# Kernel optimization log

Measured on AMD Instinct MI355X. Metric: run time of the kernel, lower is better.

## Reference

```python
import jax, jax.numpy as jnp
import numpy as np

N_NODES = 100000
N_EDGES = 1600000
IN_FEATS = 128
HIDDEN = 128
N_CLASSES = 47


def setup_inputs() -> dict:
    key = jax.random.key(0)
    ks = jax.random.split(key, 8)
    x = jax.random.normal(ks[0], (N_NODES, IN_FEATS), dtype=jnp.float32)
    edges = jax.random.randint(ks[1], (2, N_EDGES), 0, N_NODES, dtype=jnp.int32)
    W0 = jax.random.normal(ks[2], (IN_FEATS, HIDDEN), dtype=jnp.float32) * (1.0 / np.sqrt(IN_FEATS))
    b0 = jnp.zeros((HIDDEN,), dtype=jnp.float32)
    W1 = jax.random.normal(ks[3], (HIDDEN, HIDDEN), dtype=jnp.float32) * (1.0 / np.sqrt(HIDDEN))
    b1 = jnp.zeros((HIDDEN,), dtype=jnp.float32)
    Wc = jax.random.normal(ks[4], (HIDDEN, N_CLASSES), dtype=jnp.float32) * (1.0 / np.sqrt(HIDDEN))
    bc = jnp.zeros((N_CLASSES,), dtype=jnp.float32)
    return {"x": x, "edges": edges, "W0": W0, "b0": b0, "W1": W1, "b1": b1, "Wc": Wc, "bc": bc}


def reference(x, edges, W0, b0, W1, b1, Wc, bc):
    N = x.shape[0]
    src, dst = edges[0], edges[1]
    ones = jnp.ones((src.shape[0],), dtype=x.dtype)
    # symmetric 'both' normalization: out-degree for src, in-degree for dst (clamped to >=1)
    out_deg = jax.ops.segment_sum(ones, src, num_segments=N)
    in_deg = jax.ops.segment_sum(ones, dst, num_segments=N)
    c_src = jnp.maximum(out_deg, 1.0) ** -0.5  # [N]
    c_dst = jnp.maximum(in_deg, 1.0) ** -0.5   # [N]

    def graph_conv(h, W, b):
        h = (h * c_src[:, None]) @ W                       # dense transform [N, H]
        h = jax.ops.segment_sum(h[src], dst, num_segments=N)  # sparse SpMM aggregation
        h = h * c_dst[:, None] + b
        return jax.nn.relu(h)

    h = graph_conv(x, W0, b0)
    h = graph_conv(h, W1, b1)
    return h @ Wc + bc
```

## Files before the change

### kernel.cpp

```cpp
#include <hip/hip_runtime.h>
#include <hip/hip_fp16.h>


#define PB 256
#define BSHIFT 8

typedef _Float16 f16x8 __attribute__((ext_vector_type(8)));
typedef float f32x4 __attribute__((ext_vector_type(4)));


__global__ __launch_bounds__(256) void k_histo(const int* __restrict__ src, int E, int* __restrict__ dout) {
  int stride = gridDim.x * blockDim.x;
  for (int e = blockIdx.x * blockDim.x + threadIdx.x; e < E; e += stride)
    atomicAdd(&dout[src[e]], 1);
}

__global__ __launch_bounds__(256) void k_coeffs_src(const int* __restrict__ dout, float* __restrict__ c_src, int N) {
  int i = blockIdx.x * blockDim.x + threadIdx.x;
  if (i < N) c_src[i] = rsqrtf((float)max(dout[i], 1));
}


__global__ __launch_bounds__(256) void k_count(const int* __restrict__ dst, int E, int per_blk, int NB,
                                               int* __restrict__ cntT) {
  __shared__ int cnt[512];
  for (int i = threadIdx.x; i < NB; i += 256) cnt[i] = 0;
  __syncthreads();
  int e0 = blockIdx.x * per_blk, e1 = min(E, e0 + per_blk);
  for (int e = e0 + threadIdx.x; e < e1; e += 256) atomicAdd(&cnt[dst[e] >> BSHIFT], 1);
  __syncthreads();
  for (int i = threadIdx.x; i < NB; i += 256) cntT[i * PB + blockIdx.x] = cnt[i];
}

__global__ __launch_bounds__(256) void k_scanblk(const int* __restrict__ cntT, int* __restrict__ offsT,
                                                 int* __restrict__ total) {
  __shared__ int s[256];
  int b = blockIdx.x, t = threadIdx.x;
  int v = cntT[b * PB + t];
  s[t] = v;
  __syncthreads();
  for (int off = 1; off < 256; off <<= 1) {
    int x = (t >= off) ? s[t - off] : 0;
    __syncthreads();
    s[t] += x;
    __syncthreads();
  }
  offsT[b * PB + t] = s[t] - v;
  if (t == 255) total[b] = s[255];
}

__global__ __launch_bounds__(512) void k_scantot(const int* __restrict__ total, int NB, int E,
                                                 int* __restrict__ bbase, int* __restrict__ row_ptr, int N) {
  __shared__ int s[512];
  int t = threadIdx.x;
  int v = (t < NB) ? total[t] : 0;
  s[t] = v;
  __syncthreads();
  for (int off = 1; off < 512; off <<= 1) {
    int x = (t >= off) ? s[t - off] : 0;
    __syncthreads();
    s[t] += x;
    __syncthreads();
  }
  if (t < NB) bbase[t] = s[t] - v;
  if (t == 0) { bbase[NB] = E; row_ptr[N] = E; }
}


__global__ __launch_bounds__(256) void k_partition(const int* __restrict__ src, const int* __restrict__ dst,
                                                   int E, int per_blk, int NB,
                                                   const int* __restrict__ offsT, const int* __restrict__ bbase,
                                                   unsigned* __restrict__ ebuf, int src_bits) {
  __shared__ int cur[512];
  for (int i = threadIdx.x; i < NB; i += 256) cur[i] = bbase[i] + offsT[i * PB + blockIdx.x];
  __syncthreads();
  int e0 = blockIdx.x * per_blk, e1 = min(E, e0 + per_blk);
  for (int e = e0 + threadIdx.x; e < e1; e += 256) {
    int d = dst[e], s = src[e];
    int pos = atomicAdd(&cur[d >> BSHIFT], 1);
    ebuf[pos] = ((unsigned)(d & ((1 << BSHIFT) - 1)) << src_bits) | (unsigned)s;
  }
}


__global__ __launch_bounds__(256) void k_finalize(const unsigned* __restrict__ ebuf, const int* __restrict__ bbase,
                                                  int N, int src_bits, int* __restrict__ row_ptr,
                                                  float* __restrict__ c_dst, int* __restrict__ col_idx) {
  __shared__ int cnt[256];
  __shared__ int s[256];
  __shared__ int cur[256];
  int b = blockIdx.x, t = threadIdx.x;
  int r0 = bbase[b], r1 = bbase[b + 1];
  cnt[t] = 0;
  __syncthreads();
  for (int i = r0 + t; i < r1; i += 256) atomicAdd(&cnt[ebuf[i] >> src_bits], 1);
  __syncthreads();
  int v = cnt[t];
  s[t] = v;
  __syncthreads();
  for (int off = 1; off < 256; off <<= 1) {
    int x = (t >= off) ? s[t - off] : 0;
    __syncthreads();
    s[t] += x;
    __syncthreads();
  }
  int ex = s[t] - v;
  cur[t] = ex;
  int node = (b << BSHIFT) + t;
  if (node < N) {
    row_ptr[node] = r0 + ex;
    c_dst[node] = rsqrtf((float)max(v, 1));
  }
  __syncthreads();
  unsigned smask = (1u << src_bits) - 1u;
  for (int i = r0 + t; i < r1; i += 256) {
    unsigned e = ebuf[i];
    int pos = r0 + atomicAdd(&cur[e >> src_bits], 1);
    col_idx[pos] = (int)((e & smask) << 8);
  }
}


__device__ __forceinline__ f16x8 load_af(const float* arow, int off, float csc) {
  float4 a0 = *(const float4*)(arow + off);
  float4 a1 = *(const float4*)(arow + off + 4);
  f16x8 v;
  v[0] = (_Float16)(a0.x * csc);
  v[1] = (_Float16)(a0.y * csc);
  v[2] = (_Float16)(a0.z * csc);
  v[3] = (_Float16)(a0.w * csc);
  v[4] = (_Float16)(a1.x * csc);
  v[5] = (_Float16)(a1.y * csc);
  v[6] = (_Float16)(a1.z * csc);
  v[7] = (_Float16)(a1.w * csc);
  return v;
}

__device__ __forceinline__ f16x8 load_af(const __half* arow, int off, float csc) {
  f16x8 v = *(const f16x8*)(arow + off);
  _Float16 c = (_Float16)csc;
#pragma unroll
  for (int j = 0; j < 8; j++) v[j] = v[j] * c;
  return v;
}

template <typename AT>
__global__ __launch_bounds__(256) void k_gemm_mfma(const AT* __restrict__ A, const float* __restrict__ W,
                                                   const float* __restrict__ scale, __half* __restrict__ out, int N) {
  __shared__ _Float16 Wt[128][136];
  int t = threadIdx.x;
  {
    int nlow = t & 15;
    int kplow = t >> 4;
#pragma unroll
    for (int j = 0; j < 32; j++) {
      int n = nlow + 16 * (j & 7);
      int kp = kplow + 16 * (j >> 3);
      float w0 = W[(size_t)(2 * kp) * 128 + n];
      float w1 = W[(size_t)(2 * kp + 1) * 128 + n];
      __half2 h2 = __floats2half2_rn(w0, w1);
      *(__half2*)&Wt[n][2 * kp] = h2;
    }
  }
  __syncthreads();

  int wave = t >> 6;
  int lane = t & 63;
  int li = lane & 15;
  int q = lane >> 4;

#pragma unroll
  for (int s2 = 0; s2 < 2; s2++) {
    int m0 = (blockIdx.x * 2 + s2) * 128 + wave * 32;
    if (m0 >= N) break;

    int mrow[2];
    float csc[2];
    bool mok[2];
    const AT* arow[2];
#pragma unroll
    for (int s = 0; s < 2; s++) {
      mrow[s] = m0 + s * 16 + li;
      mok[s] = mrow[s] < N;
      csc[s] = mok[s] ? scale[mrow[s]] : 0.f;
      arow[s] = A + (size_t)(mok[s] ? mrow[s] : 0) * 128;
    }

    f32x4 acc[2][8];
#pragma unroll
    for (int s = 0; s < 2; s++)
#pragma unroll
      for (int nt = 0; nt < 8; nt++) acc[s][nt] = (f32x4){0.f, 0.f, 0.f, 0.f};

#pragma unroll
    for (int kc = 0; kc < 128; kc += 32) {
      f16x8 af[2];
#pragma unroll
      for (int s = 0; s < 2; s++) af[s] = load_af(arow[s], kc + q * 8, csc[s]);
#pragma unroll
      for (int nt = 0; nt < 8; nt++) {
        f16x8 wf = *(const f16x8*)&Wt[nt * 16 + li][kc + q * 8];
        acc[0][nt] = __builtin_amdgcn_mfma_f32_16x16x32_f16(wf, af[0], acc[0][nt], 0, 0, 0);
        acc[1][nt] = __builtin_amdgcn_mfma_f32_16x16x32_f16(wf, af[1], acc[1][nt], 0, 0, 0);
      }
    }

#pragma unroll
    for (int s = 0; s < 2; s++) {
      if (!mok[s]) continue;
      size_t rb = (size_t)mrow[s] * 128;
#pragma unroll
      for (int nt = 0; nt < 8; nt++) {
        __half2 p0 = __floats2half2_rn(acc[s][nt][0], acc[s][nt][1]);
        __half2 p1 = __floats2half2_rn(acc[s][nt][2], acc[s][nt][3]);
        uint2 qv;
        qv.x = *(unsigned*)&p0;
        qv.y = *(unsigned*)&p1;
        *(uint2*)&out[rb + nt * 16 + q * 4] = qv;
      }
    }
  }
}


__device__ __forceinline__ void acc_pair(float4& a, uint2 qa, uint2 qb) {
  __half2 s0 = __hadd2(*(__half2*)&qa.x, *(__half2*)&qb.x);
  __half2 s1 = __hadd2(*(__half2*)&qa.y, *(__half2*)&qb.y);
  float2 f0 = __half22float2(s0);
  float2 f1 = __half22float2(s1);
  a.x += f0.x; a.y += f0.y; a.z += f1.x; a.w += f1.y;
}

__device__ __forceinline__ void acc_one(float4& a, uint2 q) {
  float2 f0 = __half22float2(*(__half2*)&q.x);
  float2 f1 = __half22float2(*(__half2*)&q.y);
  a.x += f0.x; a.y += f0.y; a.z += f1.x; a.w += f1.y;
}

__global__ __launch_bounds__(256) void k_aggregate_h(const __half* __restrict__ hin, const int* __restrict__ rp,
                                                     const int* __restrict__ ci, const float* __restrict__ c_dst,
                                                     const float* __restrict__ bias, __half* __restrict__ hout, int N) {
  int v = blockIdx.x * 4 + (threadIdx.x >> 6);
  if (v >= N) return;
  int half_id = (threadIdx.x >> 5) & 1;
  int f4 = (threadIdx.x & 31) * 4;
  const char* hb = (const char*)hin + f4 * 2;
  int p0 = rp[v], pe = rp[v + 1];
  int mid = p0 + ((pe - p0 + 1) >> 1);
  int p = half_id ? mid : p0;
  int pend = half_id ? pe : mid;
  float4 a0 = make_float4(0.f, 0.f, 0.f, 0.f);
  float4 a1 = make_float4(0.f, 0.f, 0.f, 0.f);
  float4 a2 = make_float4(0.f, 0.f, 0.f, 0.f);
  float4 a3 = make_float4(0.f, 0.f, 0.f, 0.f);
  for (; p + 7 < pend; p += 8) {
    int u0 = ci[p];
    int u1 = ci[p + 1];
    int u2 = ci[p + 2];
    int u3 = ci[p + 3];
    int u4 = ci[p + 4];
    int u5 = ci[p + 5];
    int u6 = ci[p + 6];
    int u7 = ci[p + 7];
    uint2 q0 = *(const uint2*)(hb + (size_t)(unsigned)u0);
    uint2 q1 = *(const uint2*)(hb + (size_t)(unsigned)u1);
    uint2 q2 = *(const uint2*)(hb + (size_t)(unsigned)u2);
    uint2 q3 = *(const uint2*)(hb + (size_t)(unsigned)u3);
    uint2 q4 = *(const uint2*)(hb + (size_t)(unsigned)u4);
    uint2 q5 = *(const uint2*)(hb + (size_t)(unsigned)u5);
    uint2 q6 = *(const uint2*)(hb + (size_t)(unsigned)u6);
    uint2 q7 = *(const uint2*)(hb + (size_t)(unsigned)u7);
    acc_pair(a0, q0, q1);
    acc_pair(a1, q2, q3);
    acc_pair(a2, q4, q5);
    acc_pair(a3, q6, q7);
  }
  for (; p + 1 < pend; p += 2) {
    int u0 = ci[p];
    int u1 = ci[p + 1];
    uint2 q0 = *(const uint2*)(hb + (size_t)(unsigned)u0);
    uint2 q1 = *(const uint2*)(hb + (size_t)(unsigned)u1);
    acc_pair(a0, q0, q1);
  }
  if (p < pend) {
    uint2 q = *(const uint2*)(hb + (size_t)(unsigned)ci[p]);
    acc_one(a0, q);
  }
  a0.x += a1.x; a0.y += a1.y; a0.z += a1.z; a0.w += a1.w;
  a2.x += a3.x; a2.y += a3.y; a2.z += a3.z; a2.w += a3.w;
  a0.x += a2.x; a0.y += a2.y; a0.z += a2.z; a0.w += a2.w;
  a0.x += __shfl_xor(a0.x, 32);
  a0.y += __shfl_xor(a0.y, 32);
  a0.z += __shfl_xor(a0.z, 32);
  a0.w += __shfl_xor(a0.w, 32);
  if (half_id == 0) {
    float cd = c_dst[v];
    float4 b = *(const float4*)&bias[f4];
    float4 o;
    o.x = fmaxf(fmaf(a0.x, cd, b.x), 0.f);
    o.y = fmaxf(fmaf(a0.y, cd, b.y), 0.f);
    o.z = fmaxf(fmaf(a0.z, cd, b.z), 0.f);
    o.w = fmaxf(fmaf(a0.w, cd, b.w), 0.f);
    __half2 p0h = __floats2half2_rn(o.x, o.y);
    __half2 p1h = __floats2half2_rn(o.z, o.w);
    uint2 qv;
    qv.x = *(unsigned*)&p0h;
    qv.y = *(unsigned*)&p1h;
    *(uint2*)&hout[(size_t)v * 128 + f4] = qv;
  }
}


__global__ __launch_bounds__(256) void k_classifier(const __half* __restrict__ h, const float* __restrict__ Wc,
                                                    const float* __restrict__ bc, float* __restrict__ out, int N) {
  __shared__ float hs[256][33];
  __shared__ float Ws[32][48];
  __shared__ float bs[48];
  int t = threadIdx.x;
  int row0 = blockIdx.x * 256;
  int tc = t & 3;
  int tm = t >> 2;
  if (t < 47) bs[t] = bc[t];
  if (t == 255) bs[47] = 0.f;

  float acc[4][12];
#pragma unroll
  for (int g = 0; g < 4; g++)
#pragma unroll
    for (int j = 0; j < 12; j++) acc[g][j] = 0.f;

  for (int kb = 0; kb < 128; kb += 32) {
#pragma unroll
    for (int i = 0; i < 4; i++) {
      int f = t + i * 256;
      int r = f >> 2;
      int c8 = (f & 3) * 8;
      int g = row0 + r;
      f16x8 v;
      if (g < N) v = *(const f16x8*)&h[(size_t)g * 128 + kb + c8];
      else {
#pragma unroll
        for (int j = 0; j < 8; j++) v[j] = (_Float16)0.f;
      }
#pragma unroll
      for (int j = 0; j < 8; j++) hs[r][c8 + j] = (float)v[j];
    }
#pragma unroll
    for (int i = 0; i < 6; i++) {
      int f = t + i * 256;
      int k = f / 48;
      int c = f - k * 48;
      Ws[k][c] = (c < 47) ? Wc[(size_t)(kb + k) * 47 + c] : 0.f;
    }
    __syncthreads();
#pragma unroll 4
    for (int k = 0; k < 32; k++) {
      float4 w0 = *(const float4*)&Ws[k][tc * 12];
      float4 w1 = *(const float4*)&Ws[k][tc * 12 + 4];
      float4 w2 = *(const float4*)&Ws[k][tc * 12 + 8];
      float a0 = hs[tm][k];
      float a1 = hs[tm + 64][k];
      float a2 = hs[tm + 128][k];
      float a3 = hs[tm + 192][k];
      float a[4] = {a0, a1, a2, a3};
#pragma unroll
      for (int g = 0; g < 4; g++) {
        acc[g][0] = fmaf(a[g], w0.x, acc[g][0]);
        acc[g][1] = fmaf(a[g], w0.y, acc[g][1]);
        acc[g][2] = fmaf(a[g], w0.z, acc[g][2]);
        acc[g][3] = fmaf(a[g], w0.w, acc[g][3]);
        acc[g][4] = fmaf(a[g], w1.x, acc[g][4]);
        acc[g][5] = fmaf(a[g], w1.y, acc[g][5]);
        acc[g][6] = fmaf(a[g], w1.z, acc[g][6]);
        acc[g][7] = fmaf(a[g], w1.w, acc[g][7]);
        acc[g][8] = fmaf(a[g], w2.x, acc[g][8]);
        acc[g][9] = fmaf(a[g], w2.y, acc[g][9]);
        acc[g][10] = fmaf(a[g], w2.z, acc[g][10]);
        acc[g][11] = fmaf(a[g], w2.w, acc[g][11]);
      }
    }
    __syncthreads();
  }
#pragma unroll
  for (int g = 0; g < 4; g++) {
    int r = row0 + tm + 64 * g;
    if (r < N) {
#pragma unroll
      for (int j = 0; j < 12; j++) {
        int c = tc * 12 + j;
        if (c < 47) out[(size_t)r * 47 + c] = acc[g][j] + bs[c];
      }
    }
  }
}


extern "C" void kernel_launch(void* const* d_in, const int* in_sizes, int n_in,
                              void* d_out, int out_size, void* d_ws, size_t ws_size,
                              hipStream_t stream) {
  const float* x  = (const float*)d_in[0];
  const int* edges = (const int*)d_in[1];
  const float* W0 = (const float*)d_in[2];
  const float* b0 = (const float*)d_in[3];
  const float* W1 = (const float*)d_in[4];
  const float* b1 = (const float*)d_in[5];
  const float* Wc = (const float*)d_in[6];
  const float* bc = (const float*)d_in[7];
  float* out = (float*)d_out;

  int N = in_sizes[0] / 128;
  int E = in_sizes[1] / 2;
  const int* src = edges;
  const int* dst = edges + E;

  int NB = (N + ((1 << BSHIFT) - 1)) >> BSHIFT;
  int src_bits = 0;
  while ((1 << src_bits) < N) src_bits++;
  int per_blk = (E + PB - 1) / PB;

  char* base = (char*)d_ws;
  size_t off = 0;
  auto alloc = [&](size_t bytes) -> void* {
    void* p = base + off;
    off += (bytes + 255) & ~(size_t)255;
    return p;
  };
  float* c_src = (float*)alloc((size_t)N * 4);
  float* c_dst = (float*)alloc((size_t)N * 4);
  int* deg_out = (int*)alloc((size_t)N * 4);
  int* row_ptr = (int*)alloc((size_t)(N + 1) * 4);
  int* col_idx = (int*)alloc((size_t)E * 4);
  __half* h0h = (__half*)alloc((size_t)N * 128 * 2);
  __half* h1h = (__half*)alloc((size_t)N * 128 * 2);

  char* hb = (char*)h1h;
  unsigned* ebuf = (unsigned*)hb;            hb += (size_t)E * 4;
  int* cntT = (int*)hb;                      hb += (size_t)NB * PB * 4;
  int* offsT = (int*)hb;                     hb += (size_t)NB * PB * 4;
  int* total = (int*)hb;                     hb += (size_t)NB * 4;
  int* bbase = (int*)hb;                     hb += (size_t)(NB + 1) * 4;

  hipMemsetAsync(deg_out, 0, (size_t)N * 4, stream);
  k_histo<<<1024, 256, 0, stream>>>(src, E, deg_out);
  k_coeffs_src<<<(N + 255) / 256, 256, 0, stream>>>(deg_out, c_src, N);

  k_count<<<PB, 256, 0, stream>>>(dst, E, per_blk, NB, cntT);
  k_scanblk<<<NB, 256, 0, stream>>>(cntT, offsT, total);
  k_scantot<<<1, 512, 0, stream>>>(total, NB, E, bbase, row_ptr, N);
  k_partition<<<PB, 256, 0, stream>>>(src, dst, E, per_blk, NB, offsT, bbase, ebuf, src_bits);
  k_finalize<<<NB, 256, 0, stream>>>(ebuf, bbase, N, src_bits, row_ptr, c_dst, col_idx);

  int strips = (N + 127) / 128;
  int gblocks = (strips + 1) / 2;
  k_gemm_mfma<float><<<gblocks, 256, 0, stream>>>(x, W0, c_src, h0h, N);
  k_aggregate_h<<<(N + 3) / 4, 256, 0, stream>>>(h0h, row_ptr, col_idx, c_dst, b0, h1h, N);
  k_gemm_mfma<__half><<<gblocks, 256, 0, stream>>>(h1h, W1, c_src, h0h, N);
  k_aggregate_h<<<(N + 3) / 4, 256, 0, stream>>>(h0h, row_ptr, col_idx, c_dst, b1, h1h, N);
  k_classifier<<<(N + 255) / 256, 256, 0, stream>>>(h1h, Wc, bc, out, N);
}
```

Baseline: 409.4 us.

## Compute out-degree via bucketed partition instead of global atomic histogram

```diff
diff --git a/kernel.cpp b/kernel.cpp
--- a/kernel.cpp
+++ b/kernel.cpp
@@ -9,27 +9,23 @@
 typedef float f32x4 __attribute__((ext_vector_type(4)));
 
 
-__global__ __launch_bounds__(256) void k_histo(const int* __restrict__ src, int E, int* __restrict__ dout) {
-  int stride = gridDim.x * blockDim.x;
-  for (int e = blockIdx.x * blockDim.x + threadIdx.x; e < E; e += stride)
-    atomicAdd(&dout[src[e]], 1);
-}
-
-__global__ __launch_bounds__(256) void k_coeffs_src(const int* __restrict__ dout, float* __restrict__ c_src, int N) {
-  int i = blockIdx.x * blockDim.x + threadIdx.x;
-  if (i < N) c_src[i] = rsqrtf((float)max(dout[i], 1));
-}
-
-
-__global__ __launch_bounds__(256) void k_count(const int* __restrict__ dst, int E, int per_blk, int NB,
-                                               int* __restrict__ cntT) {
+__global__ __launch_bounds__(256) void k_count(const int* __restrict__ src, const int* __restrict__ dst,
+                                               int E, int per_blk, int NB,
+                                               int* __restrict__ cntT, int* __restrict__ cntT2) {
   __shared__ int cnt[512];
-  for (int i = threadIdx.x; i < NB; i += 256) cnt[i] = 0;
+  __shared__ int cnt2[512];
+  for (int i = threadIdx.x; i < NB; i += 256) { cnt[i] = 0; cnt2[i] = 0; }
   __syncthreads();
   int e0 = blockIdx.x * per_blk, e1 = min(E, e0 + per_blk);
-  for (int e = e0 + threadIdx.x; e < e1; e += 256) atomicAdd(&cnt[dst[e] >> BSHIFT], 1);
-  __syncthreads();
-  for (int i = threadIdx.x; i < NB; i += 256) cntT[i * PB + blockIdx.x] = cnt[i];
+  for (int e = e0 + threadIdx.x; e < e1; e += 256) {
+    atomicAdd(&cnt[dst[e] >> BSHIFT], 1);
+    atomicAdd(&cnt2[src[e] >> BSHIFT], 1);
+  }
+  __syncthreads();
+  for (int i = threadIdx.x; i < NB; i += 256) {
+    cntT[i * PB + blockIdx.x] = cnt[i];
+    cntT2[i * PB + blockIdx.x] = cnt2[i];
+  }
 }
 
 __global__ __launch_bounds__(256) void k_scanblk(const int* __restrict__ cntT, int* __restrict__ offsT,
@@ -63,22 +59,33 @@
     __syncthreads();
   }
   if (t < NB) bbase[t] = s[t] - v;
-  if (t == 0) { bbase[NB] = E; row_ptr[N] = E; }
+  if (t == 0) {
+    bbase[NB] = E;
+    if (row_ptr) row_ptr[N] = E;
+  }
 }
 
 
 __global__ __launch_bounds__(256) void k_partition(const int* __restrict__ src, const int* __restrict__ dst,
                                                    int E, int per_blk, int NB,
                                                    const int* __restrict__ offsT, const int* __restrict__ bbase,
-                                                   unsigned* __restrict__ ebuf, int src_bits) {
+                                                   const int* __restrict__ offsT2, const int* __restrict__ sbase,
+                                                   unsigned* __restrict__ ebuf, unsigned char* __restrict__ sbuf,
+                                                   int src_bits) {
   __shared__ int cur[512];
-  for (int i = threadIdx.x; i < NB; i += 256) cur[i] = bbase[i] + offsT[i * PB + blockIdx.x];
+  __shared__ int cur2[512];
+  for (int i = threadIdx.x; i < NB; i += 256) {
+    cur[i] = bbase[i] + offsT[i * PB + blockIdx.x];
+    cur2[i] = sbase[i] + offsT2[i * PB + blockIdx.x];
+  }
   __syncthreads();
   int e0 = blockIdx.x * per_blk, e1 = min(E, e0 + per_blk);
   for (int e = e0 + threadIdx.x; e < e1; e += 256) {
     int d = dst[e], s = src[e];
     int pos = atomicAdd(&cur[d >> BSHIFT], 1);
     ebuf[pos] = ((unsigned)(d & ((1 << BSHIFT) - 1)) << src_bits) | (unsigned)s;
+    int pos2 = atomicAdd(&cur2[s >> BSHIFT], 1);
+    sbuf[pos2] = (unsigned char)(s & ((1 << BSHIFT) - 1));
   }
 }
 
@@ -118,6 +125,21 @@
     int pos = r0 + atomicAdd(&cur[e >> src_bits], 1);
     col_idx[pos] = (int)((e & smask) << 8);
   }
+}
+
+
+__global__ __launch_bounds__(256) void k_finalize_src(const unsigned char* __restrict__ sbuf,
+                                                      const int* __restrict__ sbase, int N,
+                                                      float* __restrict__ c_src) {
+  __shared__ int cnt[256];
+  int b = blockIdx.x, t = threadIdx.x;
+  int r0 = sbase[b], r1 = sbase[b + 1];
+  cnt[t] = 0;
+  __syncthreads();
+  for (int i = r0 + t; i < r1; i += 256) atomicAdd(&cnt[sbuf[i]], 1);
+  __syncthreads();
+  int node = (b << BSHIFT) + t;
+  if (node < N) c_src[node] = rsqrtf((float)max(cnt[t], 1));
 }
 
 
@@ -427,7 +449,6 @@
   };
   float* c_src = (float*)alloc((size_t)N * 4);
   float* c_dst = (float*)alloc((size_t)N * 4);
-  int* deg_out = (int*)alloc((size_t)N * 4);
   int* row_ptr = (int*)alloc((size_t)(N + 1) * 4);
   int* col_idx = (int*)alloc((size_t)E * 4);
   __half* h0h = (__half*)alloc((size_t)N * 128 * 2);
@@ -435,20 +456,24 @@
 
   char* hb = (char*)h1h;
   unsigned* ebuf = (unsigned*)hb;            hb += (size_t)E * 4;
-  int* cntT = (int*)hb;                      hb += (size_t)NB * PB * 4;
-  int* offsT = (int*)hb;                     hb += (size_t)NB * PB * 4;
-  int* total = (int*)hb;                     hb += (size_t)NB * 4;
+  unsigned char* sbuf = (unsigned char*)hb;  hb += ((size_t)E + 255) & ~(size_t)255;
+  int* cntT = (int*)hb;                      hb += (size_t)2 * NB * PB * 4;
+  int* offsT = (int*)hb;                     hb += (size_t)2 * NB * PB * 4;
+  int* total = (int*)hb;                     hb += (size_t)2 * NB * 4;
   int* bbase = (int*)hb;                     hb += (size_t)(NB + 1) * 4;
-
-  hipMemsetAsync(deg_out, 0, (size_t)N * 4, stream);
-  k_histo<<<1024, 256, 0, stream>>>(src, E, deg_out);
-  k_coeffs_src<<<(N + 255) / 256, 256, 0, stream>>>(deg_out, c_src, N);
-
-  k_count<<<PB, 256, 0, stream>>>(dst, E, per_blk, NB, cntT);
-  k_scanblk<<<NB, 256, 0, stream>>>(cntT, offsT, total);
+  int* sbase = (int*)hb;                     hb += (size_t)(NB + 1) * 4;
+  int* cntT2 = cntT + (size_t)NB * PB;
+  int* offsT2 = offsT + (size_t)NB * PB;
+  int* total2 = total + NB;
+
+  k_count<<<PB, 256, 0, stream>>>(src, dst, E, per_blk, NB, cntT, cntT2);
+  k_scanblk<<<2 * NB, 256, 0, stream>>>(cntT, offsT, total);
   k_scantot<<<1, 512, 0, stream>>>(total, NB, E, bbase, row_ptr, N);
-  k_partition<<<PB, 256, 0, stream>>>(src, dst, E, per_blk, NB, offsT, bbase, ebuf, src_bits);
+  k_scantot<<<1, 512, 0, stream>>>(total2, NB, E, sbase, (int*)nullptr, N);
+  k_partition<<<PB, 256, 0, stream>>>(src, dst, E, per_blk, NB, offsT, bbase, offsT2, sbase,
+                                      ebuf, sbuf, src_bits);
   k_finalize<<<NB, 256, 0, stream>>>(ebuf, bbase, N, src_bits, row_ptr, c_dst, col_idx);
+  k_finalize_src<<<NB, 256, 0, stream>>>(sbuf, sbase, N, c_src);
 
   int strips = (N + 127) / 128;
   int gblocks = (strips + 1) / 2;
```

Result: faster. 366.9 us (-10.4%).
